# Performance work log

Hardware: AMD Instinct MI355X
Metric: run time of the kernel (lower is better)

## Reference

```python
import jax, jax.numpy as jnp
import numpy as np

N_HEAD = 12
N_EMBD = 768

def setup_inputs() -> dict:
    key = jax.random.key(0)
    k1, k2, k3 = jax.random.split(key, 3)
    B, T, C = 4, 2048, N_EMBD
    x = jax.random.normal(k1, (B, T, C), dtype=jnp.float32)
    w_attn = jax.random.normal(k2, (C, 3 * C), dtype=jnp.float32) * (C ** -0.5)
    b_attn = jnp.zeros((3 * C,), dtype=jnp.float32)
    w_proj = jax.random.normal(k3, (C, C), dtype=jnp.float32) * (C ** -0.5)
    b_proj = jnp.zeros((C,), dtype=jnp.float32)
    return {"x": x, "w_attn": w_attn, "b_attn": b_attn, "w_proj": w_proj, "b_proj": b_proj}

def reference(x, w_attn, b_attn, w_proj, b_proj):
    B, T, C = x.shape
    H = N_HEAD
    D = C // H
    qkv = x @ w_attn + b_attn  # [B,T,3C]
    q, k, v = jnp.split(qkv, 3, axis=-1)
    # [B,H,T,D]
    q = q.reshape(B, T, H, D).transpose(0, 2, 1, 3)
    k = k.reshape(B, T, H, D).transpose(0, 2, 1, 3)
    v = v.reshape(B, T, H, D).transpose(0, 2, 1, 3)
    # NOTE: source scales by n_embd**-0.5, not head_dim**-0.5
    scores = jnp.einsum('bhqd,bhkd->bhqk', q, k) * (C ** -0.5)
    causal = jnp.triu(jnp.ones((T, T), dtype=bool), k=1)  # True above diagonal
    scores = jnp.where(causal, -jnp.inf, scores)
    attn = jax.nn.softmax(scores, axis=-1)
    out = jnp.einsum('bhqk,bhkd->bhqd', attn, v)  # [B,H,T,D]
    out = out.transpose(0, 2, 1, 3).reshape(B, T, C)
    return out @ w_proj + b_proj
```

## Files before the change

### kernel.cpp

```cpp
#include <hip/hip_runtime.h>
#include <cstdint>
#include <cstddef>

typedef __attribute__((ext_vector_type(8))) short bf8_t;
typedef __attribute__((ext_vector_type(4))) float f4_t;
typedef __attribute__((ext_vector_type(16))) float f16v_t;
typedef __attribute__((ext_vector_type(2))) unsigned u2_t;
typedef __attribute__((ext_vector_type(4))) unsigned u4_t;

#define DEVFN static __device__ __forceinline__
#define MFMA16(a, b, c) __builtin_amdgcn_mfma_f32_16x16x32_bf16(a, b, c, 0, 0, 0)
#define MFMA32(a, b, c) __builtin_amdgcn_mfma_f32_32x32x16_bf16(a, b, c, 0, 0, 0)

constexpr float kQscale = 0.05205877317700523f;

DEVFN short f2bs(float f) {
  uint32_t u = __builtin_bit_cast(uint32_t, f);
  u = (u + 0x7FFFu + ((u >> 16) & 1u)) >> 16;
  return (short)(uint16_t)u;
}

DEVFN unsigned cvtpk(float lo, float hi) {
  unsigned r;
  asm("v_cvt_pk_bf16_f32 %0, %1, %2" : "=v"(r) : "v"(lo), "v"(hi));
  return r;
}

DEVFN float red2_sum(float v) { return v + __shfl_xor(v, 32, 64); }

DEVFN void gload16(const void* g, void* l) {
  __builtin_amdgcn_global_load_lds(
      (const __attribute__((address_space(1))) void*)g,
      (__attribute__((address_space(3))) void*)l, 16, 0, 0);
}

__global__ __launch_bounds__(256) void prep(const float* __restrict__ x,
                                            short* __restrict__ xb,
                                            const float* __restrict__ w_attn,
                                            short* __restrict__ wat,
                                            const float* __restrict__ w_proj,
                                            short* __restrict__ wpt) {
  __shared__ float tile[32][33];
  const int blk = blockIdx.x, tid = threadIdx.x;
  if (blk < 3072) {
    const int i = blk * 256 + tid;
    const f4_t* p = (const f4_t*)x + (size_t)i * 2;
    f4_t a = p[0], b = p[1];
    bf8_t h;
    h[0] = f2bs(a[0]); h[1] = f2bs(a[1]); h[2] = f2bs(a[2]); h[3] = f2bs(a[3]);
    h[4] = f2bs(b[0]); h[5] = f2bs(b[1]); h[6] = f2bs(b[2]); h[7] = f2bs(b[3]);
    *((bf8_t*)xb + i) = h;
    return;
  }
  const float* w;
  short* wT;
  int N, n0, k0;
  if (blk < 4800) {
    const int bb = blk - 3072;
    w = w_attn; wT = wat; N = 2304;
    n0 = (bb % 72) << 5; k0 = (bb / 72) << 5;
  } else {
    const int bb = blk - 4800;
    w = w_proj; wT = wpt; N = 768;
    n0 = (bb % 24) << 5; k0 = (bb / 24) << 5;
  }
  const int tx = tid & 31, ty = tid >> 5;
#pragma unroll
  for (int i = 0; i < 4; ++i)
    tile[ty * 4 + i][tx] = w[(size_t)(k0 + ty * 4 + i) * N + n0 + tx];
  __syncthreads();
#pragma unroll
  for (int i = 0; i < 4; ++i)
    wT[(size_t)(n0 + ty * 4 + i) * 768 + k0 + tx] = f2bs(tile[tx][ty * 4 + i]);
}

template <int EPI, int BN, int NW>
__global__ __launch_bounds__(NW * 64) void gemm_bf16(
    const short* __restrict__ A, const short* __restrict__ Bt,
    const float* __restrict__ bias, float* __restrict__ outF,
    short* __restrict__ qb, short* __restrict__ kb, short* __restrict__ vtb,
    int Mdim, int Ndim, int Kdim) {
  constexpr int NT = NW * 64;
  constexpr int WCN = NW / 2;
  constexpr int WNW = BN / WCN;
  constexpr int NI = WNW / 16;
  constexpr int ACH = 16 / NW;
  constexpr int BCH = BN / (8 * NW);
  __shared__ char smem[32768 + 2 * (BN << 7)];
  const int nbx = gridDim.x;
  const int bid = blockIdx.x + nbx * blockIdx.y;
  const int xcd = bid & 7, slot = bid >> 3;
  const int mp = xcd + ((slot / nbx) << 3);
  const int np = slot % nbx;
  const int m0 = mp << 7, n0 = np * BN;
  const int tid = threadIdx.x;
  const int lane = tid & 63, wid = tid >> 6;
  const int wr = wid / WCN, wc = wid % WCN;
  const int g = lane >> 4, cl = lane & 15;
  const int ldb = Kdim << 1;

  f4_t acc[4][NI];
#pragma unroll
  for (int mi = 0; mi < 4; ++mi)
#pragma unroll
    for (int ni = 0; ni < NI; ++ni) acc[mi][ni] = (f4_t){0.f, 0.f, 0.f, 0.f};

  const char* ga = (const char*)(A + (size_t)m0 * Kdim);
  const char* gb = (const char*)(Bt + (size_t)n0 * Kdim);
  auto stage = [&](int b, int ks) {
    const int k0b = ks << 7;
    char* Ab = smem + (b << 14);
    char* Bb = smem + 32768 + b * (BN << 7);
#pragma unroll
    for (int i = 0; i < ACH; ++i) {
      const int doff = (wid * ACH + i) << 10;
      const int boff = doff + lane * 16;
      const int row = boff >> 7;
      const int src = row * ldb + k0b + ((boff & 127) ^ ((row & 7) << 4));
      gload16(ga + src, Ab + doff);
    }
#pragma unroll
    for (int i = 0; i < BCH; ++i) {
      const int doff = (wid * BCH + i) << 10;
      const int boff = doff + lane * 16;
      const int row = boff >> 7;
      const int src = row * ldb + k0b + ((boff & 127) ^ ((row & 7) << 4));
      gload16(gb + src, Bb + doff);
    }
  };

  const int nk = Kdim >> 6;
  stage(0, 0);
  __syncthreads();

  int cur = 0;
  for (int ks = 0; ks < nk; ++ks) {
    const int ksn = (ks + 1 < nk) ? ks + 1 : ks;
    stage(cur ^ 1, ksn);
    const char* Ab = smem + (cur << 14);
    const char* Bb = smem + 32768 + cur * (BN << 7);
#pragma unroll
    for (int kk = 0; kk < 2; ++kk) {
      bf8_t af[4], bfv[NI];
#pragma unroll
      for (int mi = 0; mi < 4; ++mi) {
        int lrow = (wr << 6) + (mi << 4) + cl;
        af[mi] = *(const bf8_t*)&Ab[(lrow << 7) + ((((kk << 2) + g) ^ (lrow & 7)) << 4)];
      }
#pragma unroll
      for (int ni = 0; ni < NI; ++ni) {
        int lrow = wc * WNW + (ni << 4) + cl;
        bfv[ni] = *(const bf8_t*)&Bb[(lrow << 7) + ((((kk << 2) + g) ^ (lrow & 7)) << 4)];
      }
#pragma unroll
      for (int mi = 0; mi < 4; ++mi)
#pragma unroll
        for (int ni = 0; ni < NI; ++ni)
          acc[mi][ni] = MFMA16(af[mi], bfv[ni], acc[mi][ni]);
    }
    __syncthreads();
    cur ^= 1;
  }

  if constexpr (EPI == 1) {
#pragma unroll
    for (int ni = 0; ni < NI; ++ni) {
      const int n = n0 + wc * WNW + (ni << 4) + cl;
      const float bv = bias[n];
#pragma unroll
      for (int mi = 0; mi < 4; ++mi)
#pragma unroll
        for (int r = 0; r < 4; ++r) {
          const int m = m0 + (wr << 6) + (mi << 4) + (g << 2) + r;
          outF[(size_t)m * 768 + n] = acc[mi][ni][r] + bv;
        }
    }
  } else {
    short* T = (short*)smem;
    const int sec = n0 / 768;
    const float qs = (sec == 0) ? kQscale : 1.0f;
#pragma unroll
    for (int ni = 0; ni < NI; ++ni) {
      const int colT = wc * WNW + (ni << 4) + cl;
      const float bv = bias[n0 + colT];
#pragma unroll
      for (int mi = 0; mi < 4; ++mi)
#pragma unroll
        for (int r = 0; r < 4; ++r) {
          const int row = (wr << 6) + (mi << 4) + (g << 2) + r;
          const int colS = ((((colT >> 3) ^ ((row >> 3) & 7)) << 3) | (colT & 7));
          T[row * 132 + colS] = f2bs((acc[mi][ni][r] + bv) * qs);
        }
    }
    __syncthreads();
    if (sec < 2) {
      short* dst0 = (sec == 0) ? qb : kb;
      const int tl = tid & 127;
      const int hh2 = (tid >> 7) & 1;
      const int half = tid >> 8;
      constexpr int JN = (NT == 256) ? 8 : 4;
      const int m = m0 + tl, b = m >> 11, t = m & 2047;
      const int hh = ((n0 - sec * 768) >> 6) + hh2;
      short* dst = dst0 + (size_t)(b * 12 + hh) * 131072 + (size_t)t * 64 + half * 32;
      const int rsw = (tl >> 3) & 7;
#pragma unroll
      for (int j = 0; j < JN; ++j) {
        const int gj = (hh2 << 3) + (half << 2) + j;
        *(bf8_t*)(dst + j * 8) =
            *(const bf8_t*)(T + tl * 132 + ((gj ^ rsw) << 3));
      }
    } else {
      const int chunk = tid & 15;
      constexpr int DLS = NT >> 4;
      const int m = m0 + (chunk << 3);
      const int b = m >> 11, t = m & 2047;
#pragma unroll
      for (int c8 = 0; c8 < 128 / DLS; ++c8) {
        const int dl = (tid >> 4) + c8 * DLS;
        const int nloc = n0 - 1536 + dl;
        const int hh = nloc >> 6, d = nloc & 63;
        const int gsw = ((dl >> 3) ^ (chunk & 7)) << 3;
        bf8_t tmp;
#pragma unroll
        for (int j = 0; j < 8; ++j)
          tmp[j] = T[((chunk << 3) + j) * 132 + gsw + (dl & 7)];
        *(bf8_t*)(vtb + (size_t)(b * 12 + hh) * 131072 + (size_t)d * 2048 + t) = tmp;
      }
    }
  }
}

__global__ __launch_bounds__(256, 2) void attn_fwd(const short* __restrict__ Q,
                                                   const short* __restrict__ K,
                                                   const short* __restrict__ Vt,
                                                   short* __restrict__ O) {
  __shared__ char kv_lds[2][32768];
  const int tid = threadIdx.x;
  const int lane = tid & 63, wid = tid >> 6;
  const int blk = blockIdx.x;
  const int bh = blk % 48;
  const int qg = 15 - blk / 48;
  const int qt = (qg << 2) + wid;
  const int q0 = qt << 5;
  const int col = lane & 31, hi = lane >> 5;

  const short* Qb = Q + (size_t)bh * 131072;
  const short* Kb = K + (size_t)bh * 131072;
  const short* Vb = Vt + (size_t)bh * 131072;

  bf8_t qf[4];
#pragma unroll
  for (int dc = 0; dc < 4; ++dc)
    qf[dc] = *(const bf8_t*)(Qb + (size_t)(q0 + col) * 64 + dc * 16 + hi * 8);

  const f16v_t zf = {0.f,0.f,0.f,0.f,0.f,0.f,0.f,0.f,0.f,0.f,0.f,0.f,0.f,0.f,0.f,0.f};
  f16v_t o0 = zf, o1 = zf;
  float ls[4] = {0.f, 0.f, 0.f, 0.f};

  const int nt = qg + 1;
  const int kxor = (col & 7) << 4;

  auto stage = [&](int b, int kcs) {
    char* buf = &kv_lds[b][0];
    if (wid < 2) {
      const char* g = (const char*)(Kb + (size_t)kcs * 64);
#pragma unroll
      for (int i = 0; i < 8; ++i) {
        const int doff = (wid << 13) + (i << 10);
        const int boff = doff + lane * 16;
        const int src = boff ^ (((boff >> 7) & 7) << 4);
        gload16(g + src, buf + doff);
      }
    } else {
      const char* g = (const char*)Vb + (size_t)kcs * 2;
#pragma unroll
      for (int i = 0; i < 8; ++i) {
        const int doff = ((wid - 2) << 13) + (i << 10);
        const int boff = doff + lane * 16;
        const int row = boff >> 8;
        const int src = row * 4096 + ((boff & 255) ^ ((row & 7) << 4));
        gload16(g + src, buf + 16384 + doff);
      }
    }
  };

  stage(0, 0);
  __syncthreads();

  int cur = 0;
  for (int st = 0; st < nt; ++st) {
    int kcn = (st + 1) << 7;
    if (kcn > 1920) kcn = 1920;
    stage(cur ^ 1, kcn);

#pragma unroll
    for (int h = 0; h < 2; ++h) {
      const int kc = (st << 7) + (h << 6);
      if (kc < q0 + 32) {
        const char* Kl = &kv_lds[cur][h << 13];
        const char* Vl = &kv_lds[cur][16384];
        f16v_t s0 = zf, s1 = zf;
#pragma unroll
        for (int dc = 0; dc < 4; ++dc) {
          const int fo = (dc * 32 + hi * 16) ^ kxor;
          bf8_t k0 = *(const bf8_t*)(Kl + col * 128 + fo);
          bf8_t k1 = *(const bf8_t*)(Kl + (32 + col) * 128 + fo);
          __builtin_amdgcn_s_setprio(1);
          s0 = MFMA32(k0, qf[dc], s0);
          s1 = MFMA32(k1, qf[dc], s1);
          __builtin_amdgcn_s_setprio(0);
        }
        if (kc + 63 > q0) {
          const int qq = q0 + col;
#pragma unroll
          for (int r = 0; r < 16; ++r) {
            const int kb_ = kc + (r & 3) + 8 * (r >> 2) + 4 * hi;
            if (kb_ > qq) s0[r] = -1e30f;
            if (kb_ + 32 > qq) s1[r] = -1e30f;
          }
        }
#pragma unroll
        for (int r = 0; r < 16; ++r) {
          s0[r] = __builtin_amdgcn_exp2f(s0[r]);
          s1[r] = __builtin_amdgcn_exp2f(s1[r]);
        }
#pragma unroll
        for (int r = 0; r < 4; ++r)
          ls[r] += ((s0[r] + s0[r + 4]) + (s0[r + 8] + s0[r + 12])) +
                   ((s1[r] + s1[r + 4]) + (s1[r + 8] + s1[r + 12]));
#pragma unroll
        for (int c = 0; c < 4; ++c) {
          const int b8 = (c & 1) * 8;
          float p0, p1, p2, p3, p4, p5, p6, p7;
          if (c < 2) {
            p0 = s0[b8+0]; p1 = s0[b8+1]; p2 = s0[b8+2]; p3 = s0[b8+3];
            p4 = s0[b8+4]; p5 = s0[b8+5]; p6 = s0[b8+6]; p7 = s0[b8+7];
          } else {
            p0 = s1[b8+0]; p1 = s1[b8+1]; p2 = s1[b8+2]; p3 = s1[b8+3];
            p4 = s1[b8+4]; p5 = s1[b8+5]; p6 = s1[b8+6]; p7 = s1[b8+7];
          }
          unsigned w0 = cvtpk(p0, p1), w1 = cvtpk(p2, p3);
          unsigned w2 = cvtpk(p4, p5), w3 = cvtpk(p6, p7);
          u2_t ra = __builtin_amdgcn_permlane32_swap(w0, w2, false, false);
          u2_t rb = __builtin_amdgcn_permlane32_swap(w1, w3, false, false);
          const bf8_t pf = __builtin_bit_cast(bf8_t, (u4_t){ra[0], rb[0], ra[1], rb[1]});
          const int vo = ((h << 7) + c * 32 + hi * 16) ^ kxor;
          bf8_t v0 = *(const bf8_t*)(Vl + col * 256 + vo);
          bf8_t v1 = *(const bf8_t*)(Vl + (32 + col) * 256 + vo);
          __builtin_amdgcn_s_setprio(1);
          o0 = MFMA32(v0, pf, o0);
          o1 = MFMA32(v1, pf, o1);
          __builtin_amdgcn_s_setprio(0);
        }
      }
    }
    __syncthreads();
    cur ^= 1;
  }

  const float l = red2_sum((ls[0] + ls[1]) + (ls[2] + ls[3]));
  const float rl = 1.0f / l;
  const int b_ = bh / 12, hh = bh % 12;
  short* Op = O + (size_t)b_ * 2048 * 768 + (size_t)(q0 + col) * 768 + hh * 64;
#pragma unroll
  for (int rq = 0; rq < 4; ++rq) {
    u2_t w0, w1;
    w0[0] = cvtpk(o0[4*rq+0] * rl, o0[4*rq+1] * rl);
    w0[1] = cvtpk(o0[4*rq+2] * rl, o0[4*rq+3] * rl);
    w1[0] = cvtpk(o1[4*rq+0] * rl, o1[4*rq+1] * rl);
    w1[1] = cvtpk(o1[4*rq+2] * rl, o1[4*rq+3] * rl);
    *(u2_t*)(Op + rq * 8 + hi * 4) = w0;
    *(u2_t*)(Op + 32 + rq * 8 + hi * 4) = w1;
  }
}

extern "C" void kernel_launch(void* const* d_in, const int* in_sizes, int n_in,
                              void* d_out, int out_size, void* d_ws, size_t ws_size,
                              hipStream_t stream) {
  const float* x      = (const float*)d_in[0];
  const float* w_attn = (const float*)d_in[1];
  const float* b_attn = (const float*)d_in[2];
  const float* w_proj = (const float*)d_in[3];
  const float* b_proj = (const float*)d_in[4];
  float* out = (float*)d_out;

  const size_t QSZ = (size_t)4 * 12 * 2048 * 64;
  short* ws  = (short*)d_ws;
  short* qb  = ws;
  short* kb  = qb + QSZ;
  short* vtb = kb + QSZ;
  short* xb  = vtb + QSZ;
  short* ob  = xb;
  short* wat = xb + QSZ;
  short* wpt = wat + (size_t)2304 * 768;

  prep<<<5376, 256, 0, stream>>>(x, xb, w_attn, wat, w_proj, wpt);

  gemm_bf16<0, 128, 8><<<dim3(18, 64), 512, 0, stream>>>(xb, wat, b_attn, nullptr,
                                                         qb, kb, vtb, 8192, 2304, 768);
  attn_fwd<<<768, 256, 0, stream>>>(qb, kb, vtb, ob);
  gemm_bf16<1, 64, 8><<<dim3(12, 64), 512, 0, stream>>>(ob, wpt, b_proj, out,
                                                        nullptr, nullptr, nullptr, 8192, 768, 768);
}
```

Baseline: 123.1 us.

## Single-buffer the B tile in the bf16 GEMM, preloading B fragments to registers

The GEMM keeps the A tile double-buffered in LDS but now holds the B tile in a single buffer. Each iteration first reads all B fragments and the first A fragment into registers. It then synchronises and issues the next-step global-to-LDS loads before running the MFMAs. This lowers the block's LDS footprint, which may allow more resident blocks per CU. The cost is an extra barrier per k-step and more live vector registers, which could reduce occupancy or overlap instead.

```diff
diff --git a/kernel.cpp b/kernel.cpp
--- a/kernel.cpp
+++ b/kernel.cpp
@@ -86,7 +86,7 @@
   constexpr int NI = WNW / 16;
   constexpr int ACH = 16 / NW;
   constexpr int BCH = BN / (8 * NW);
-  __shared__ char smem[32768 + 2 * (BN << 7)];
+  __shared__ char smem[32768 + (BN << 7)];
   const int nbx = gridDim.x;
   const int bid = blockIdx.x + nbx * blockIdx.y;
   const int xcd = bid & 7, slot = bid >> 3;
@@ -107,10 +107,9 @@
 
   const char* ga = (const char*)(A + (size_t)m0 * Kdim);
   const char* gb = (const char*)(Bt + (size_t)n0 * Kdim);
-  auto stage = [&](int b, int ks) {
+  auto stageA = [&](int b, int ks) {
     const int k0b = ks << 7;
     char* Ab = smem + (b << 14);
-    char* Bb = smem + 32768 + b * (BN << 7);
 #pragma unroll
     for (int i = 0; i < ACH; ++i) {
       const int doff = (wid * ACH + i) << 10;
@@ -119,6 +118,10 @@
       const int src = row * ldb + k0b + ((boff & 127) ^ ((row & 7) << 4));
       gload16(ga + src, Ab + doff);
     }
+  };
+  auto stageB = [&](int ks) {
+    const int k0b = ks << 7;
+    char* Bb = smem + 32768;
 #pragma unroll
     for (int i = 0; i < BCH; ++i) {
       const int doff = (wid * BCH + i) << 10;
@@ -130,34 +133,47 @@
   };
 
   const int nk = Kdim >> 6;
-  stage(0, 0);
+  stageA(0, 0);
+  stageB(0);
   __syncthreads();
 
   int cur = 0;
   for (int ks = 0; ks < nk; ++ks) {
     const int ksn = (ks + 1 < nk) ? ks + 1 : ks;
-    stage(cur ^ 1, ksn);
     const char* Ab = smem + (cur << 14);
-    const char* Bb = smem + 32768 + cur * (BN << 7);
-#pragma unroll
-    for (int kk = 0; kk < 2; ++kk) {
-      bf8_t af[4], bfv[NI];
-#pragma unroll
-      for (int mi = 0; mi < 4; ++mi) {
-        int lrow = (wr << 6) + (mi << 4) + cl;
-        af[mi] = *(const bf8_t*)&Ab[(lrow << 7) + ((((kk << 2) + g) ^ (lrow & 7)) << 4)];
-      }
+    const char* Bb = smem + 32768;
+    bf8_t bfv[2][NI], af0[4];
+#pragma unroll
+    for (int kk = 0; kk < 2; ++kk)
 #pragma unroll
       for (int ni = 0; ni < NI; ++ni) {
         int lrow = wc * WNW + (ni << 4) + cl;
-        bfv[ni] = *(const bf8_t*)&Bb[(lrow << 7) + ((((kk << 2) + g) ^ (lrow & 7)) << 4)];
-      }
-#pragma unroll
-      for (int mi = 0; mi < 4; ++mi)
-#pragma unroll
-        for (int ni = 0; ni < NI; ++ni)
-          acc[mi][ni] = MFMA16(af[mi], bfv[ni], acc[mi][ni]);
-    }
+        bfv[kk][ni] = *(const bf8_t*)&Bb[(lrow << 7) + ((((kk << 2) + g) ^ (lrow & 7)) << 4)];
+      }
+#pragma unroll
+    for (int mi = 0; mi < 4; ++mi) {
+      int lrow = (wr << 6) + (mi << 4) + cl;
+      af0[mi] = *(const bf8_t*)&Ab[(lrow << 7) + (((g) ^ (lrow & 7)) << 4)];
+    }
+    __syncthreads();
+    stageA(cur ^ 1, ksn);
+    stageB(ksn);
+#pragma unroll
+    for (int mi = 0; mi < 4; ++mi)
+#pragma unroll
+      for (int ni = 0; ni < NI; ++ni)
+        acc[mi][ni] = MFMA16(af0[mi], bfv[0][ni], acc[mi][ni]);
+    bf8_t af1[4];
+#pragma unroll
+    for (int mi = 0; mi < 4; ++mi) {
+      int lrow = (wr << 6) + (mi << 4) + cl;
+      af1[mi] = *(const bf8_t*)&Ab[(lrow << 7) + (((4 + g) ^ (lrow & 7)) << 4)];
+    }
+#pragma unroll
+    for (int mi = 0; mi < 4; ++mi)
+#pragma unroll
+      for (int ni = 0; ni < NI; ++ni)
+        acc[mi][ni] = MFMA16(af1[mi], bfv[1][ni], acc[mi][ni]);
     __syncthreads();
     cur ^= 1;
   }
```

Result: faster. 114.8 us (-6.7%).
